# Kernel tuning notes

Measured on AMD Instinct MI355X. Metric: run time of the kernel, lower is better.

Reference implementation:

```python
import jax, jax.numpy as jnp
import numpy as np
import math

B, S, D, H = 16, 1024, 512, 8
DPH = D // H


def _lorentz_linear(x, W, b, log_scale):
    # LorentzLinear.forward: linear map then project onto hyperboloid
    x = x @ W.T + b
    time = jax.nn.sigmoid(x[..., :1]) * jnp.exp(log_scale) + 1.0 + 1e-4
    rest = x[..., 1:]
    sq = jnp.clip(jnp.sum(rest * rest, axis=-1, keepdims=True), 1e-8, None)
    scale = (time * time - 1.0) / sq
    return jnp.concatenate([time, rest * jnp.sqrt(scale)], axis=-1)


def setup_inputs() -> dict:
    key = jax.random.key(0)
    ks = jax.random.split(key, 16)
    stdv = 1.0 / math.sqrt(D)

    def mk_w(k):
        W = jax.random.uniform(k, (D, D), minval=-stdv, maxval=stdv, dtype=jnp.float32)
        return W.at[:, 0].set(0.0)  # reset_parameters zeroes column 0

    inp = {
        'key': jax.random.normal(ks[0], (B, S, D), dtype=jnp.float32),
        'value': jax.random.normal(ks[1], (B, S, D), dtype=jnp.float32),
        'query': jax.random.normal(ks[2], (B, S, D), dtype=jnp.float32),
        'Wq': mk_w(ks[3]), 'bq': jnp.zeros((D,), jnp.float32), 'lsq': jnp.asarray(math.log(10.0), jnp.float32),
        'Wk': mk_w(ks[4]), 'bk': jnp.zeros((D,), jnp.float32), 'lsk': jnp.asarray(math.log(10.0), jnp.float32),
        'Wv': mk_w(ks[5]), 'bv': jnp.zeros((D,), jnp.float32), 'lsv': jnp.asarray(math.log(10.0), jnp.float32),
        'attn_scale': jnp.asarray([math.sqrt(D)], jnp.float32),
        'attn_bias': jnp.zeros((), jnp.float32),
    }
    return inp


def reference(key, value, query, Wq, bq, lsq, Wk, bk, lsk, Wv, bv, lsv, attn_scale, attn_bias):
    q = _lorentz_linear(query, Wq, bq, lsq)  # [B,S,D]
    k = _lorentz_linear(key, Wk, bk, lsk)
    v = _lorentz_linear(value, Wv, bv, lsv)

    def shape(x):
        b, s, _ = x.shape
        return x.reshape(b, s, H, DPH).transpose(0, 2, 1, 3)  # [B,H,S,dph]

    q, k, v = shape(q), shape(k), shape(v)

    # Minkowski signature (-,+,...,+) on the per-head feature dim
    sgn = jnp.concatenate([-jnp.ones((1,), q.dtype), jnp.ones((DPH - 1,), q.dtype)])

    # attn = (2 + 2 * cinner(q, k)) / scale + bias  (no softmax, per source)
    attn = (2.0 + 2.0 * jnp.einsum('bhqd,bhkd->bhqk', q * sgn, k)) / attn_scale + attn_bias

    # mid_point: ave = attn @ v, then normalize by sqrt(|<ave,ave>_L|)
    ave = jnp.einsum('bhqk,bhkd->bhqd', attn, v)
    inner = jnp.sum(ave * ave * sgn, axis=-1, keepdims=True)  # Lorentz inner product
    denom = jnp.sqrt(jnp.clip(jnp.abs(inner), 1e-8, None))
    ctx = ave / denom  # [B,H,S,dph]

    b = ctx.shape[0]
    return ctx.transpose(0, 2, 1, 3).reshape(b, -1, H * DPH)  # [B,S,D]
```

## Files before the change

### kernel.cpp

```cpp
#include <hip/hip_runtime.h>
#include <stdint.h>

#define B_    16
#define S_    1024
#define D_    512
#define H_    8
#define DPH_  64
#define MTOT  (B_*S_)

typedef __attribute__((ext_vector_type(8))) short  short8;
typedef __attribute__((ext_vector_type(4))) float  float4v;
typedef __attribute__((ext_vector_type(4))) ushort u16x4;

__device__ inline float bf2f(ushort u) {
    union { uint32_t u; float f; } c; c.u = ((uint32_t)u) << 16; return c.f;
}
__device__ inline ushort f2bf(float f) {
    union { float f; uint32_t u; } c; c.f = f;
    uint32_t x = c.u;
    return (ushort)((x + 0x7fffu + ((x >> 16) & 1u)) >> 16);
}
__device__ inline bool mode_f32(const void* as) {
    return ((const ushort*)as)[0] == (ushort)0x04F3u;
}

typedef __attribute__((address_space(1))) uint32_t glob_u32;
typedef __attribute__((address_space(3))) uint32_t lds_u32;
__device__ __forceinline__ void gload16(const ushort* g, ushort* l) {
    __builtin_amdgcn_global_load_lds((glob_u32*)g, (lds_u32*)l, 16, 0, 0);
}

__global__ __launch_bounds__(256) void convert_w(
    const void* __restrict__ Wq, const void* __restrict__ Wk,
    const void* __restrict__ Wv, const void* __restrict__ as_flag,
    ushort* __restrict__ WP, float4* __restrict__ zb)
{
    const int idx = blockIdx.x * 256 + threadIdx.x;
    if (idx < 145408) zb[idx] = (float4){0.f, 0.f, 0.f, 0.f};
    if (!mode_f32(as_flag)) return;
    const int z   = idx >> 16;
    const int off = idx & 65535;
    const float* W = z == 0 ? (const float*)Wq
                   : z == 1 ? (const float*)Wk : (const float*)Wv;
    const float4 v = ((const float4*)W)[off];
    ushort* whi = WP + (size_t)z * 524288;
    ushort* wlo = whi + 262144;
    u16x4 h, l;
    #pragma unroll
    for (int q = 0; q < 4; ++q) {
        const float f = (&v.x)[q];
        const ushort hi = f2bf(f);
        h[q] = hi;
        l[q] = f2bf(f - bf2f(hi));
    }
    *(u16x4*)&whi[off * 4] = h;
    *(u16x4*)&wlo[off * 4] = l;
}

__global__ __launch_bounds__(256) void gemm_proj(
    const void* __restrict__ Xq, const void* __restrict__ Xk, const void* __restrict__ Xv,
    const void* __restrict__ Wq, const void* __restrict__ Wk, const void* __restrict__ Wv,
    const void* __restrict__ bq, const void* __restrict__ bk, const void* __restrict__ bv,
    const void* __restrict__ as_flag, const ushort* __restrict__ Wplanes,
    float* __restrict__ Yq, float* __restrict__ Yk, float* __restrict__ Yv,
    float* __restrict__ RowY0, float* __restrict__ RowSq)
{
    const int z = blockIdx.z;
    const void* X    = z == 0 ? Xq : (z == 1 ? Xk : Xv);
    const void* W    = z == 0 ? Wq : (z == 1 ? Wk : Wv);
    const void* bias = z == 0 ? bq : (z == 1 ? bk : bv);
    float*      Y    = z == 0 ? Yq : (z == 1 ? Yk : Yv);
    const bool  f32  = mode_f32(as_flag);

    const int m0   = blockIdx.x * 128;
    const int n0   = blockIdx.y * 128;
    const int tid  = threadIdx.x;
    const int lane = tid & 63;
    const int w    = tid >> 6;
    const int wm   = w >> 1, wn = w & 1;

    __shared__ __align__(16) char smem[32768];
    ushort* s16 = (ushort*)smem;

    float4v acc[4][4];
    #pragma unroll
    for (int i = 0; i < 4; ++i)
        #pragma unroll
        for (int j = 0; j < 4; ++j)
            acc[i][j] = (float4v){0.f, 0.f, 0.f, 0.f};

    const int fr = lane & 15;
    const int fk = (lane >> 4) * 8;

    if (!f32) {
        int offA[4], offB[4];
        #pragma unroll
        for (int i = 0; i < 4; ++i) offA[i] = (wm * 64 + i * 16 + fr) * 32 + fk;
        #pragma unroll
        for (int j = 0; j < 4; ++j) offB[j] = (wn * 64 + j * 16 + fr) * 32 + fk;
        const ushort* Xu = (const ushort*)X;
        const ushort* Wu = (const ushort*)W;
        const int rsub = lane >> 2;
        const int cg   = (lane & 3) * 8;
        const ushort* gA0 = Xu + (size_t)(m0 + w * 16      + rsub) * D_ + cg;
        const ushort* gA1 = Xu + (size_t)(m0 + w * 16 + 64 + rsub) * D_ + cg;
        const ushort* gB0 = Wu + (size_t)(n0 + w * 16      + rsub) * D_ + cg;
        const ushort* gB1 = Wu + (size_t)(n0 + w * 16 + 64 + rsub) * D_ + cg;
        const int dA0 = w * 512;
        const int dA1 = 2048 + w * 512;

        gload16(gA0, &s16[dA0]);
        gload16(gA1, &s16[dA1]);
        gload16(gB0, &s16[4096 + dA0]);
        gload16(gB1, &s16[4096 + dA1]);
        __syncthreads();

        int cur = 0;
        for (int kt = 32; kt < D_; kt += 32) {
            const int nb = (cur ^ 1) * 8192;
            gload16(gA0 + kt, &s16[nb + dA0]);
            gload16(gA1 + kt, &s16[nb + dA1]);
            gload16(gB0 + kt, &s16[nb + 4096 + dA0]);
            gload16(gB1 + kt, &s16[nb + 4096 + dA1]);
            const ushort* bb = &s16[cur * 8192];
            short8 ah[4], bh[4];
            #pragma unroll
            for (int i = 0; i < 4; ++i) ah[i] = *(const short8*)&bb[offA[i]];
            #pragma unroll
            for (int j = 0; j < 4; ++j) bh[j] = *(const short8*)&bb[4096 + offB[j]];
            #pragma unroll
            for (int i = 0; i < 4; ++i)
                #pragma unroll
                for (int j = 0; j < 4; ++j)
                    acc[i][j] = __builtin_amdgcn_mfma_f32_16x16x32_bf16(ah[i], bh[j], acc[i][j], 0, 0, 0);
            __syncthreads();
            cur ^= 1;
        }
        {
            const ushort* bb = &s16[cur * 8192];
            short8 ah[4], bh[4];
            #pragma unroll
            for (int i = 0; i < 4; ++i) ah[i] = *(const short8*)&bb[offA[i]];
            #pragma unroll
            for (int j = 0; j < 4; ++j) bh[j] = *(const short8*)&bb[4096 + offB[j]];
            #pragma unroll
            for (int i = 0; i < 4; ++i)
                #pragma unroll
                for (int j = 0; j < 4; ++j)
                    acc[i][j] = __builtin_amdgcn_mfma_f32_16x16x32_bf16(ah[i], bh[j], acc[i][j], 0, 0, 0);
        }
    } else {
        const float*  Xf   = (const float*)X;
        const ushort* WhiZ = Wplanes + (size_t)z * 524288;
        const ushort* WloZ = WhiZ + 262144;

        int wrow[4], wc4[4], woff[4];
        #pragma unroll
        for (int it = 0; it < 4; ++it) {
            const int c = tid + it * 256;
            const int row = c >> 3, c4 = (c & 7) * 4;
            wrow[it] = row; wc4[it] = c4;
            woff[it] = row * 32 + ((((c4 >> 3) + (row >> 1)) & 3) << 3) + (c4 & 4);
        }
        const int rsub  = lane >> 2;
        const int sG    = lane & 3;
        const int rowB0 = w * 16 + rsub;
        const int rowB1 = 64 + w * 16 + rsub;
        const int g0 = ((sG - (rowB0 >> 1)) & 3) * 8;
        const int g1 = ((sG - (rowB1 >> 1)) & 3) * 8;
        const ushort* pBh0 = WhiZ + (size_t)(n0 + rowB0) * D_ + g0;
        const ushort* pBh1 = WhiZ + (size_t)(n0 + rowB1) * D_ + g1;
        const ushort* pBl0 = WloZ + (size_t)(n0 + rowB0) * D_ + g0;
        const ushort* pBl1 = WloZ + (size_t)(n0 + rowB1) * D_ + g1;
        ushort* dBh0 = &s16[8192  + w * 512];
        ushort* dBh1 = &s16[8192  + 2048 + w * 512];
        ushort* dBl0 = &s16[12288 + w * 512];
        ushort* dBl1 = &s16[12288 + 2048 + w * 512];

        int offAs[4], offBs[4];
        #pragma unroll
        for (int i = 0; i < 4; ++i) {
            const int row = wm * 64 + i * 16 + fr;
            offAs[i] = row * 32 + ((((fk >> 3) + (row >> 1)) & 3) << 3);
        }
        #pragma unroll
        for (int j = 0; j < 4; ++j) {
            const int row = wn * 64 + j * 16 + fr;
            offBs[j] = row * 32 + ((((fk >> 3) + (row >> 1)) & 3) << 3);
        }

        for (int kt = 0; kt < D_; kt += 32) {
            __syncthreads();
            gload16(pBh0 + kt, dBh0);
            gload16(pBh1 + kt, dBh1);
            gload16(pBl0 + kt, dBl0);
            gload16(pBl1 + kt, dBl1);
            #pragma unroll
            for (int it = 0; it < 4; ++it) {
                const float4 fa = *(const float4*)&Xf[(size_t)(m0 + wrow[it]) * D_ + kt + wc4[it]];
                u16x4 ah4, al4;
                #pragma unroll
                for (int q = 0; q < 4; ++q) {
                    const float fav = (&fa.x)[q];
                    union { float f; uint32_t u; } cc; cc.f = fav;
                    const ushort ha = (ushort)(cc.u >> 16);
                    ah4[q] = ha;
                    al4[q] = f2bf(fav - bf2f(ha));
                }
                *(u16x4*)&s16[woff[it]]        = ah4;
                *(u16x4*)&s16[4096 + woff[it]] = al4;
            }
            __syncthreads();
            short8 ah[4], al[4], bh[4], bl[4];
            #pragma unroll
            for (int i = 0; i < 4; ++i) {
                ah[i] = *(const short8*)&s16[offAs[i]];
                al[i] = *(const short8*)&s16[4096 + offAs[i]];
            }
            #pragma unroll
            for (int j = 0; j < 4; ++j) {
                bh[j] = *(const short8*)&s16[8192  + offBs[j]];
                bl[j] = *(const short8*)&s16[12288 + offBs[j]];
            }
            #pragma unroll
            for (int i = 0; i < 4; ++i)
                #pragma unroll
                for (int j = 0; j < 4; ++j) {
                    acc[i][j] = __builtin_amdgcn_mfma_f32_16x16x32_bf16(ah[i], bh[j], acc[i][j], 0, 0, 0);
                    acc[i][j] = __builtin_amdgcn_mfma_f32_16x16x32_bf16(al[i], bh[j], acc[i][j], 0, 0, 0);
                    acc[i][j] = __builtin_amdgcn_mfma_f32_16x16x32_bf16(ah[i], bl[j], acc[i][j], 0, 0, 0);
                }
        }
    }

    __syncthreads();
    float* sRS = (float*)smem;
    const int er = lane >> 4;
    float bvf[4];
    #pragma unroll
    for (int j = 0; j < 4; ++j) {
        const int n = n0 + wn * 64 + j * 16 + fr;
        bvf[j] = f32 ? ((const float*)bias)[n] : bf2f(((const ushort*)bias)[n]);
    }
    #pragma unroll
    for (int i = 0; i < 4; ++i)
        #pragma unroll
        for (int r = 0; r < 4; ++r) {
            const int row = wm * 64 + i * 16 + er * 4 + r;
            const int m = m0 + row;
            float rsum = 0.f;
            #pragma unroll
            for (int j = 0; j < 4; ++j) {
                const int n = n0 + wn * 64 + j * 16 + fr;
                const float y = acc[i][j][r] + bvf[j];
                Y[(size_t)m * D_ + n] = y;
                if (n != 0) rsum += y * y;
            }
            rsum += __shfl_xor(rsum, 1, 64);
            rsum += __shfl_xor(rsum, 2, 64);
            rsum += __shfl_xor(rsum, 4, 64);
            rsum += __shfl_xor(rsum, 8, 64);
            if (fr == 0) sRS[wn * 128 + row] = rsum;
            if (blockIdx.y == 0 && wn == 0 && fr == 0)
                RowY0[z * MTOT + m] = acc[i][0][r] + bvf[0];
        }
    __syncthreads();
    if (tid < 128) {
        const float v = sRS[tid] + sRS[128 + tid];
        atomicAdd(&RowSq[z * MTOT + m0 + tid], v);
    }
}

__global__ __launch_bounds__(256) void kv_k(
    const float* __restrict__ Yk, const float* __restrict__ Yv,
    const float* __restrict__ T, const float* __restrict__ A,
    const void* __restrict__ lk, const void* __restrict__ lv,
    const void* __restrict__ as_flag,
    float* __restrict__ KV, float* __restrict__ Vs)
{
    const int bh = blockIdx.x;
    const int sp = blockIdx.y;
    const int b = bh >> 3, h = bh & 7;
    const int t = threadIdx.x;
    const int td = t & 15, te = t >> 4;
    const bool f32 = mode_f32(as_flag);

    __shared__ float sK[16][64];
    __shared__ float sV[16][64];
    __shared__ float4 sTA[128];

    const int r  = t >> 4;
    const int c4 = (t & 15) * 4;
    const size_t mbase = (size_t)b * S_ + (size_t)sp * 128;

    if (t < 128) {
        const float elsk = expf(f32 ? ((const float*)lk)[0] : bf2f(((const ushort*)lk)[0]));
        const float elsv = expf(f32 ? ((const float*)lv)[0] : bf2f(((const ushort*)lv)[0]));
        const size_t m = mbase + t;
        const float y0k = T[MTOT + m],     sqk = A[MTOT + m];
        const float y0v = T[2 * MTOT + m], sqv = A[2 * MTOT + m];
        const float tk = (1.f / (1.f + expf(-y0k))) * elsk + 1.0f + 1e-4f;
        const float tv = (1.f / (1.f + expf(-y0v))) * elsv + 1.0f + 1e-4f;
        sTA[t] = (float4){tk, sqrtf((tk * tk - 1.0f) / fmaxf(sqk, 1e-8f)),
                          tv, sqrtf((tv * tv - 1.0f) / fmaxf(sqv, 1e-8f))};
    }

    float acc[4][4] = {};
    float vs[4] = {0.f, 0.f, 0.f, 0.f};

    for (int sc = 0; sc < 128; sc += 16) {
        const size_t m = mbase + sc + r;
        __syncthreads();
        float4 kr = *(const float4*)&Yk[m * D_ + h * DPH_ + c4];
        float4 vr = *(const float4*)&Yv[m * D_ + h * DPH_ + c4];
        const float4 ta = sTA[sc + r];
        kr.x *= ta.y; kr.y *= ta.y; kr.z *= ta.y; kr.w *= ta.y;
        vr.x *= ta.w; vr.y *= ta.w; vr.z *= ta.w; vr.w *= ta.w;
        if (h == 0 && c4 == 0) { kr.x = ta.x; vr.x = ta.z; }
        *(float4*)&sK[r][c4] = kr;
        *(float4*)&sV[r][c4] = vr;
        __syncthreads();
        #pragma unroll
        for (int rr = 0; rr < 16; ++rr) {
            const float4 k4 = *(const float4*)&sK[rr][te * 4];
            const float4 v4 = *(const float4*)&sV[rr][td * 4];
            #pragma unroll
            for (int i = 0; i < 4; ++i)
                #pragma unroll
                for (int j = 0; j < 4; ++j)
                    acc[i][j] += (&k4.x)[i] * (&v4.x)[j];
            #pragma unroll
            for (int j = 0; j < 4; ++j) vs[j] += (&v4.x)[j];
        }
    }

    #pragma unroll
    for (int i = 0; i < 4; ++i)
        #pragma unroll
        for (int j = 0; j < 4; ++j)
            atomicAdd(&KV[(size_t)bh * 4096 + (te * 4 + i) * 64 + td * 4 + j],
                      acc[i][j]);
    if (te == 0) {
        #pragma unroll
        for (int j = 0; j < 4; ++j)
            atomicAdd(&Vs[(size_t)bh * 64 + td * 4 + j], vs[j]);
    }
}

__global__ __launch_bounds__(256) void ave_norm(
    const float* __restrict__ Yq, const float* __restrict__ T, const float* __restrict__ A,
    const float* __restrict__ KV, const float* __restrict__ Vs,
    const void* __restrict__ lq,
    const void* __restrict__ as_ptr, const void* __restrict__ ab_ptr,
    void* __restrict__ outp)
{
    const int bh = blockIdx.x >> 3;
    const int st = blockIdx.x & 7;
    const int b = bh >> 3, h = bh & 7;
    const int s0 = st * 128;
    const int t = threadIdx.x;
    const int lane = t & 63;
    const int w = t >> 6;
    const bool f32 = mode_f32(as_ptr);

    __shared__ ushort sKVh[64 * 64];
    __shared__ ushort sKVl[64 * 64];
    __shared__ ushort sQh[128 * 64];
    __shared__ ushort sQl[128 * 64];
    __shared__ float  sVs[64];
    __shared__ float2 sTA2[128];

    if (t < 128) {
        const float elsq = expf(f32 ? ((const float*)lq)[0] : bf2f(((const ushort*)lq)[0]));
        const size_t m = (size_t)b * S_ + s0 + t;
        const float y0 = T[m], sq = A[m];
        const float tim = (1.f / (1.f + expf(-y0))) * elsq + 1.0f + 1e-4f;
        sTA2[t] = (float2){tim, sqrtf((tim * tim - 1.0f) / fmaxf(sq, 1e-8f))};
    }
    __syncthreads();

    #pragma unroll
    for (int i = 0; i < 16; ++i) {
        const int idx = t + i * 256;
        const int e = idx >> 6, d = idx & 63;
        const float v = KV[(size_t)bh * 4096 + idx];
        const ushort hi = f2bf(v);
        const int off = d * 64 + (e ^ ((d & 7) << 3));
        sKVh[off] = hi;
        sKVl[off] = f2bf(v - bf2f(hi));
    }
    if (t < 64) sVs[t] = Vs[(size_t)bh * 64 + t];
    #pragma unroll
    for (int i = 0; i < 8; ++i) {
        const int idx = t + i * 256;
        const int row = idx >> 4, c4 = (idx & 15) * 4;
        const size_t m = (size_t)b * S_ + s0 + row;
        const float4 q4 = *(const float4*)&Yq[m * D_ + h * DPH_ + c4];
        const float2 ta = sTA2[row];
        u16x4 qh, ql;
        #pragma unroll
        for (int q = 0; q < 4; ++q) {
            const int col = c4 + q;
            float val = (&q4.x)[q] * ta.y;
            if (h == 0 && col == 0) val = ta.x;
            if (col == 0) val = -val;
            const ushort hi = f2bf(val);
            qh[q] = hi;
            ql[q] = f2bf(val - bf2f(hi));
        }
        const int c4s = ((((c4 >> 3) ^ (row & 7)) << 3) | (c4 & 4));
        *(u16x4*)&sQh[row * 64 + c4s] = qh;
        *(u16x4*)&sQl[row * 64 + c4s] = ql;
    }
    __syncthreads();

    const float asv = f32 ? ((const float*)as_ptr)[0] : bf2f(((const ushort*)as_ptr)[0]);
    const float abv = f32 ? ((const float*)ab_ptr)[0] : bf2f(((const ushort*)ab_ptr)[0]);
    const float c1f = 2.0f / asv;
    const float c0f = c1f + abv;

    const int fr = lane & 15, fq = lane >> 4;

    float4v acc[2][4];
    #pragma unroll
    for (int mi = 0; mi < 2; ++mi)
        #pragma unroll
        for (int j = 0; j < 4; ++j)
            acc[mi][j] = (float4v){0.f, 0.f, 0.f, 0.f};

    #pragma unroll
    for (int kk = 0; kk < 2; ++kk) {
        const int ko = kk * 32 + fq * 8;
        short8 ah[2], al[2], bh4[4], bl4[4];
        #pragma unroll
        for (int mi = 0; mi < 2; ++mi) {
            const int rowA = w * 32 + mi * 16 + fr;
            const int koA  = (((ko >> 3) ^ (rowA & 7)) << 3);
            ah[mi] = *(const short8*)&sQh[rowA * 64 + koA];
            al[mi] = *(const short8*)&sQl[rowA * 64 + koA];
        }
        #pragma unroll
        for (int j = 0; j < 4; ++j) {
            const int rowB = j * 16 + fr;
            const int koB  = (((ko >> 3) ^ (rowB & 7)) << 3);
            bh4[j] = *(const short8*)&sKVh[rowB * 64 + koB];
            bl4[j] = *(const short8*)&sKVl[rowB * 64 + koB];
        }
        #pragma unroll
        for (int mi = 0; mi < 2; ++mi)
            #pragma unroll
            for (int j = 0; j < 4; ++j) {
                acc[mi][j] = __builtin_amdgcn_mfma_f32_16x16x32_bf16(ah[mi], bh4[j], acc[mi][j], 0, 0, 0);
                acc[mi][j] = __builtin_amdgcn_mfma_f32_16x16x32_bf16(ah[mi], bl4[j], acc[mi][j], 0, 0, 0);
                acc[mi][j] = __builtin_amdgcn_mfma_f32_16x16x32_bf16(al[mi], bh4[j], acc[mi][j], 0, 0, 0);
            }
    }

    #pragma unroll
    for (int mi = 0; mi < 2; ++mi) {
        float avev[4][4];
        float part[4] = {0.f, 0.f, 0.f, 0.f};
        #pragma unroll
        for (int j = 0; j < 4; ++j) {
            const float vsn = sVs[j * 16 + fr];
            #pragma unroll
            for (int r = 0; r < 4; ++r) {
                const float a = c1f * acc[mi][j][r] + c0f * vsn;
                avev[j][r] = a;
                part[r] += (j == 0 && fr == 0) ? -(a * a) : (a * a);
            }
        }
        #pragma unroll
        for (int off = 1; off < 16; off <<= 1)
            #pragma unroll
            for (int r = 0; r < 4; ++r)
                part[r] += __shfl_xor(part[r], off, 64);
        float rd[4];
        #pragma unroll
        for (int r = 0; r < 4; ++r)
            rd[r] = 1.0f / sqrtf(fmaxf(fabsf(part[r]), 1e-8f));
        #pragma unroll
        for (int j = 0; j < 4; ++j)
            #pragma unroll
            for (int r = 0; r < 4; ++r) {
                const int srow = s0 + w * 32 + mi * 16 + fq * 4 + r;
                const size_t oidx = ((size_t)b * S_ + srow) * D_ + h * DPH_ + j * 16 + fr;
                const float cv = avev[j][r] * rd[r];
                if (f32) ((float*)outp)[oidx] = cv;
                else     ((ushort*)outp)[oidx] = f2bf(cv);
            }
    }
}

extern "C" void kernel_launch(void* const* d_in, const int* in_sizes, int n_in,
                              void* d_out, int out_size, void* d_ws, size_t ws_size,
                              hipStream_t stream)
{
    const void* key    = d_in[0];
    const void* value  = d_in[1];
    const void* query  = d_in[2];
    const void* Wq     = d_in[3];
    const void* bq     = d_in[4];
    const void* lsq    = d_in[5];
    const void* Wk     = d_in[6];
    const void* bk     = d_in[7];
    const void* lsk    = d_in[8];
    const void* Wv     = d_in[9];
    const void* bv     = d_in[10];
    const void* lsv    = d_in[11];
    const void* ascale = d_in[12];
    const void* abias  = d_in[13];

    char* ws = (char*)d_ws;
    float*  Yq    = (float*)(ws + 0);
    float*  Yk    = (float*)(ws + 33554432);
    float*  Yv    = (float*)(ws + 67108864);
    float*  T     = (float*)(ws + 100663296);
    float*  Alpha = (float*)(ws + 100859904);
    float*  KV    = (float*)(ws + 101056512);
    float*  Vs    = (float*)(ws + 103153664);
    ushort* WPL   = (ushort*)d_out;

    convert_w<<<768, 256, 0, stream>>>(Wq, Wk, Wv, ascale, WPL,
                                       (float4*)(ws + 100859904));

    gemm_proj<<<dim3(MTOT / 128, D_ / 128, 3), 256, 0, stream>>>(
        query, key, value, Wq, Wk, Wv, bq, bk, bv, ascale, WPL,
        Yq, Yk, Yv, T, Alpha);

    kv_k<<<dim3(B_ * H_, 8), 256, 0, stream>>>(
        Yk, Yv, T, Alpha, lsk, lsv, ascale, KV, Vs);

    ave_norm<<<B_ * H_ * (S_ / 128), 256, 0, stream>>>(
        Yq, T, Alpha, KV, Vs, lsq, ascale, abias, d_out);
}
```

Baseline: 317.1 us.

## Double-buffer LDS in fp32 projection GEMM to overlap loads with MFMA

The fp32 path of the projection GEMM now uses two LDS buffers. The next K-tile's weight global_load_lds and X loads are issued before the current tile's MFMAs, and the split-bf16 conversion is written after them, so one barrier per iteration replaces two. The low-part rounding also switches from round-to-nearest to truncation, which saves a few ALU ops but slightly reduces the accuracy of the bf16x3 emulation. LDS use doubles to 64KB, which may lower occupancy.

After: 304.2 us. -4.1%, faster.

```diff
diff --git a/kernel.cpp b/kernel.cpp
--- a/kernel.cpp
+++ b/kernel.cpp
@@ -19,6 +19,10 @@
     union { float f; uint32_t u; } c; c.f = f;
     uint32_t x = c.u;
     return (ushort)((x + 0x7fffu + ((x >> 16) & 1u)) >> 16);
+}
+__device__ inline ushort f2bf_trunc(float f) {
+    union { float f; uint32_t u; } c; c.f = f;
+    return (ushort)(c.u >> 16);
 }
 __device__ inline bool mode_f32(const void* as) {
     return ((const ushort*)as)[0] == (ushort)0x04F3u;
@@ -79,7 +83,7 @@
     const int w    = tid >> 6;
     const int wm   = w >> 1, wn = w & 1;
 
-    __shared__ __align__(16) char smem[32768];
+    __shared__ __align__(16) char smem[65536];
     ushort* s16 = (ushort*)smem;
 
     float4v acc[4][4];
@@ -172,10 +176,10 @@
         const ushort* pBh1 = WhiZ + (size_t)(n0 + rowB1) * D_ + g1;
         const ushort* pBl0 = WloZ + (size_t)(n0 + rowB0) * D_ + g0;
         const ushort* pBl1 = WloZ + (size_t)(n0 + rowB1) * D_ + g1;
-        ushort* dBh0 = &s16[8192  + w * 512];
-        ushort* dBh1 = &s16[8192  + 2048 + w * 512];
-        ushort* dBl0 = &s16[12288 + w * 512];
-        ushort* dBl1 = &s16[12288 + 2048 + w * 512];
+        const int dB0 = 8192  + w * 512;
+        const int dB1 = 8192  + 2048 + w * 512;
+        const int dL0 = 12288 + w * 512;
+        const int dL1 = 12288 + 2048 + w * 512;
 
         int offAs[4], offBs[4];
         #pragma unroll
@@ -189,38 +193,56 @@
             offBs[j] = row * 32 + ((((fk >> 3) + (row >> 1)) & 3) << 3);
         }
 
-        for (int kt = 0; kt < D_; kt += 32) {
-            __syncthreads();
-            gload16(pBh0 + kt, dBh0);
-            gload16(pBh1 + kt, dBh1);
-            gload16(pBl0 + kt, dBl0);
-            gload16(pBl1 + kt, dBl1);
+        gload16(pBh0, &s16[dB0]);
+        gload16(pBh1, &s16[dB1]);
+        gload16(pBl0, &s16[dL0]);
+        gload16(pBl1, &s16[dL1]);
+        {
+            float4 fa0[4];
+            #pragma unroll
+            for (int it = 0; it < 4; ++it)
+                fa0[it] = *(const float4*)&Xf[(size_t)(m0 + wrow[it]) * D_ + wc4[it]];
             #pragma unroll
             for (int it = 0; it < 4; ++it) {
-                const float4 fa = *(const float4*)&Xf[(size_t)(m0 + wrow[it]) * D_ + kt + wc4[it]];
                 u16x4 ah4, al4;
                 #pragma unroll
                 for (int q = 0; q < 4; ++q) {
-                    const float fav = (&fa.x)[q];
-                    union { float f; uint32_t u; } cc; cc.f = fav;
-                    const ushort ha = (ushort)(cc.u >> 16);
+                    const float fav = (&fa0[it].x)[q];
+                    const ushort ha = f2bf_trunc(fav);
                     ah4[q] = ha;
-                    al4[q] = f2bf(fav - bf2f(ha));
+                    al4[q] = f2bf_trunc(fav - bf2f(ha));
                 }
                 *(u16x4*)&s16[woff[it]]        = ah4;
                 *(u16x4*)&s16[4096 + woff[it]] = al4;
             }
-            __syncthreads();
+        }
+        __syncthreads();
+
+        int cur = 0;
+        for (int kt = 0; kt < D_; kt += 32) {
+            const bool more = (kt + 32 < D_);
+            const int nb = (cur ^ 1) * 16384;
+            float4 fa[4];
+            if (more) {
+                gload16(pBh0 + kt + 32, &s16[nb + dB0]);
+                gload16(pBh1 + kt + 32, &s16[nb + dB1]);
+                gload16(pBl0 + kt + 32, &s16[nb + dL0]);
+                gload16(pBl1 + kt + 32, &s16[nb + dL1]);
+                #pragma unroll
+                for (int it = 0; it < 4; ++it)
+                    fa[it] = *(const float4*)&Xf[(size_t)(m0 + wrow[it]) * D_ + kt + 32 + wc4[it]];
+            }
+            const ushort* bb = &s16[cur * 16384];
             short8 ah[4], al[4], bh[4], bl[4];
             #pragma unroll
             for (int i = 0; i < 4; ++i) {
-                ah[i] = *(const short8*)&s16[offAs[i]];
-                al[i] = *(const short8*)&s16[4096 + offAs[i]];
+                ah[i] = *(const short8*)&bb[offAs[i]];
+                al[i] = *(const short8*)&bb[4096 + offAs[i]];
             }
             #pragma unroll
             for (int j = 0; j < 4; ++j) {
-                bh[j] = *(const short8*)&s16[8192  + offBs[j]];
-                bl[j] = *(const short8*)&s16[12288 + offBs[j]];
+                bh[j] = *(const short8*)&bb[8192  + offBs[j]];
+                bl[j] = *(const short8*)&bb[12288 + offBs[j]];
             }
             #pragma unroll
             for (int i = 0; i < 4; ++i)
@@ -230,6 +252,23 @@
                     acc[i][j] = __builtin_amdgcn_mfma_f32_16x16x32_bf16(al[i], bh[j], acc[i][j], 0, 0, 0);
                     acc[i][j] = __builtin_amdgcn_mfma_f32_16x16x32_bf16(ah[i], bl[j], acc[i][j], 0, 0, 0);
                 }
+            if (more) {
+                #pragma unroll
+                for (int it = 0; it < 4; ++it) {
+                    u16x4 ah4, al4;
+                    #pragma unroll
+                    for (int q = 0; q < 4; ++q) {
+                        const float fav = (&fa[it].x)[q];
+                        const ushort ha = f2bf_trunc(fav);
+                        ah4[q] = ha;
+                        al4[q] = f2bf_trunc(fav - bf2f(ha));
+                    }
+                    *(u16x4*)&s16[nb + woff[it]]        = ah4;
+                    *(u16x4*)&s16[nb + 4096 + woff[it]] = al4;
+                }
+            }
+            __syncthreads();
+            cur ^= 1;
         }
     }
 
```
